# Optimization experiments

Hardware: AMD Instinct MI355X
Metric: run time of the kernel (lower is better)

Reference implementation:

```python
import jax, jax.numpy as jnp
import numpy as np
from jax import lax

SCALES = (1, 4, 16, 64)
EPS = 1e-5
B, S, D, H, R, FF = 4, 1024, 512, 8, 4, 2048
C = D // len(SCALES)  # channels per temporal scale


def _ln(x, g, b):
    mu = jnp.mean(x, -1, keepdims=True)
    var = jnp.mean(jnp.square(x - mu), -1, keepdims=True)
    return (x - mu) * lax.rsqrt(var + EPS) * g + b


def _interp_linear(y, L_out):
    # y: [B, C, L_in]; torch F.interpolate(mode='linear', align_corners=False)
    L_in = y.shape[-1]
    if L_in == L_out:
        return y
    pos = (jnp.arange(L_out, dtype=jnp.float32) + 0.5) * (L_in / L_out) - 0.5
    pos = jnp.clip(pos, 0.0, L_in - 1)
    lo = jnp.floor(pos).astype(jnp.int32)
    hi = jnp.minimum(lo + 1, L_in - 1)
    w = (pos - lo.astype(jnp.float32))
    return y[..., lo] * (1.0 - w) + y[..., hi] * w


def _conv1d(x, w, b, stride):
    # x: [B, Cin, L], w: [Cout, Cin, K]
    y = lax.conv_general_dilated(x, w, window_strides=(stride,), padding='VALID',
                                 dimension_numbers=('NCH', 'OIH', 'NCH'))
    return y + b[None, :, None]


def setup_inputs() -> dict:
    key = jax.random.key(0)
    ks = jax.random.split(key, 40)
    n = lambda k, shp, s=0.02: jax.random.normal(k, shp, jnp.float32) * s
    inp = {}
    inp['x'] = jax.random.normal(ks[0], (B, S, D), jnp.float32)
    inp['resource_mask'] = jax.random.randint(ks[1], (B, S), 0, R, jnp.int32)
    inp['attention_mask'] = jnp.ones((B, S), jnp.int32)
    inp['wq'] = n(ks[2], (D, D)); inp['bq'] = jnp.zeros((D,), jnp.float32)
    inp['wk'] = n(ks[3], (D, D)); inp['bk'] = jnp.zeros((D,), jnp.float32)
    inp['wv'] = n(ks[4], (D, D)); inp['bv'] = jnp.zeros((D,), jnp.float32)
    inp['wo'] = n(ks[5], (D, D)); inp['bo'] = jnp.zeros((D,), jnp.float32)
    inp['rbias'] = jax.random.normal(ks[6], (H, R, R), jnp.float32)
    for i, sc in enumerate(SCALES):
        inp[f'cw{i}'] = n(ks[7 + i], (C, D, sc))
        inp[f'cb{i}'] = jnp.zeros((C,), jnp.float32)
    inp['fw'] = n(ks[12], (D, D)); inp['fb'] = jnp.zeros((D,), jnp.float32)
    inp['ltg'] = jnp.ones((D,), jnp.float32); inp['ltb'] = jnp.zeros((D,), jnp.float32)
    inp['n1g'] = jnp.ones((D,), jnp.float32); inp['n1b'] = jnp.zeros((D,), jnp.float32)
    inp['n2g'] = jnp.ones((D,), jnp.float32); inp['n2b'] = jnp.zeros((D,), jnp.float32)
    inp['fw1'] = n(ks[13], (FF, D)); inp['fb1'] = jnp.zeros((FF,), jnp.float32)
    inp['fw2'] = n(ks[14], (D, FF)); inp['fb2'] = jnp.zeros((D,), jnp.float32)
    inp['n3g'] = jnp.ones((D,), jnp.float32); inp['n3b'] = jnp.zeros((D,), jnp.float32)
    return inp


def reference(x, resource_mask, attention_mask, wq, bq, wk, bk, wv, bv, wo, bo, rbias,
              cw0, cb0, cw1, cb1, cw2, cb2, cw3, cb3, fw, fb, ltg, ltb,
              n1g, n1b, n2g, n2b, fw1, fb1, fw2, fb2, n3g, n3b):
    b_, s_, d_ = x.shape
    dk = d_ // H
    # --- ResourceAwareAttention (dropout = identity in eval) ---
    q = (x @ wq.T + bq).reshape(b_, s_, H, dk).transpose(0, 2, 1, 3)
    k = (x @ wk.T + bk).reshape(b_, s_, H, dk).transpose(0, 2, 1, 3)
    v = (x @ wv.T + bv).reshape(b_, s_, H, dk).transpose(0, 2, 1, 3)
    scores = jnp.einsum('bhid,bhjd->bhij', q, k) / jnp.sqrt(jnp.float32(dk))
    # vectorized resource-bias gather: bias[b,h,i,j] = rbias[h, rm[b,i], rm[b,j]]
    idx_h = jnp.arange(H)[None, :, None, None]
    idx_i = resource_mask[:, None, :, None]
    idx_j = resource_mask[:, None, None, :]
    scores = scores + rbias[idx_h, idx_i, idx_j]
    scores = jnp.where(attention_mask[:, None, None, :] == 0, -1e9, scores)
    attn = jax.nn.softmax(scores, axis=-1)
    o = jnp.einsum('bhij,bhjd->bhid', attn, v).transpose(0, 2, 1, 3).reshape(b_, s_, d_)
    attn_out = o @ wo.T + bo
    x = _ln(x + attn_out, n1g, n1b)
    # --- MultiScaleTemporalEncoder ---
    xc = x.transpose(0, 2, 1)  # [B, D, S]
    convs = ((cw0, cb0), (cw1, cb1), (cw2, cb2), (cw3, cb3))
    outs = []
    for sc, (w, bb) in zip(SCALES, convs):
        y = _conv1d(xc, w, bb, sc)  # [B, C, S/sc]
        outs.append(_interp_linear(y, s_))
    ms = jnp.concatenate(outs, axis=1).transpose(0, 2, 1)  # [B, S, D]
    fused = ms @ fw.T + fb
    temporal = _ln(x + fused, ltg, ltb)
    x = _ln(x + temporal, n2g, n2b)
    # --- FFN ---
    ff = jax.nn.relu(x @ fw1.T + fb1) @ fw2.T + fb2
    return _ln(x + ff, n3g, n3b)
```

## Files before the change

kernel.cpp:

```cpp
#include <hip/hip_runtime.h>
#include <math.h>

constexpr int B_ = 4, S_ = 1024, D_ = 512, H_ = 8, FF_ = 2048;
constexpr int DK_ = 64;
constexpr int C_ = 128;
constexpr int QKVLD = 1536;

typedef __bf16 bf16x8 __attribute__((ext_vector_type(8)));
typedef __bf16 bf16x4 __attribute__((ext_vector_type(4)));
typedef short short4v __attribute__((ext_vector_type(4)));
typedef float floatx4 __attribute__((ext_vector_type(4)));

__device__ __forceinline__ void g2l16(const __bf16* g, __bf16* l) {
  __builtin_amdgcn_global_load_lds(
      (__attribute__((address_space(1))) void*)(unsigned long long)g,
      (__attribute__((address_space(3))) void*)(unsigned int)(unsigned long long)l,
      16, 0, 0);
}

template <bool OUTBF16, bool RELU, bool WRITEVT>
__global__ __launch_bounds__(256, 2) void mgemm(
    const __bf16* __restrict__ A, const __bf16* __restrict__ W,
    const float* __restrict__ bias, void* __restrict__ Yv,
    int M, int N, int K, int ldY, __bf16* __restrict__ VT) {
  __shared__ __bf16 As[2][128 * 64];
  __shared__ __bf16 Bs[2][128 * 64];
  const int tid = threadIdx.x;
  const int wave = tid >> 6, lane = tid & 63;
  const int bm = blockIdx.y * 128, bn = blockIdx.x * 128;

  const int rsub = lane >> 3;
  const int gch = ((lane & 7) ^ rsub) * 8;
  const __bf16* gA = A + (size_t)(bm + wave * 32 + rsub) * K + gch;
  const __bf16* gB = W + (size_t)(bn + wave * 32 + rsub) * K + gch;

  const int mrow = lane & 15, g4 = lane >> 4;
  const int rsw = mrow & 7;
  const int wm = (wave & 1) * 64, wn = (wave >> 1) * 64;

  floatx4 acc[4][4];
#pragma unroll
  for (int mi = 0; mi < 4; mi++)
#pragma unroll
    for (int ni = 0; ni < 4; ni++) acc[mi][ni] = (floatx4){0.f, 0.f, 0.f, 0.f};

  const int nk = K >> 6;
  auto stage = [&](int buf, int kt) {
    const __bf16* ga = gA + (size_t)kt * 64;
    const __bf16* gb = gB + (size_t)kt * 64;
    __bf16* la = &As[buf][wave * 32 * 64];
    __bf16* lb = &Bs[buf][wave * 32 * 64];
#pragma unroll
    for (int i = 0; i < 4; i++) {
      g2l16(ga + (size_t)(i * 8) * K, la + i * 8 * 64);
      g2l16(gb + (size_t)(i * 8) * K, lb + i * 8 * 64);
    }
  };

  stage(0, 0);
  int cur = 0;
  for (int kk = 0; kk < nk; kk++) {
    __syncthreads();
    if (kk + 1 < nk) stage(cur ^ 1, kk + 1);
    const __bf16* Ab = As[cur];
    const __bf16* Bb = Bs[cur];
#pragma unroll
    for (int c = 0; c < 2; c++) {
      const int pc = (((c * 4 + g4) ^ rsw)) * 8;
      bf16x8 af[4], bfr[4];
#pragma unroll
      for (int mi = 0; mi < 4; mi++)
        af[mi] = *(const bf16x8*)(Ab + (wm + mi * 16 + mrow) * 64 + pc);
#pragma unroll
      for (int ni = 0; ni < 4; ni++)
        bfr[ni] = *(const bf16x8*)(Bb + (wn + ni * 16 + mrow) * 64 + pc);
#pragma unroll
      for (int mi = 0; mi < 4; mi++)
#pragma unroll
        for (int ni = 0; ni < 4; ni++)
          acc[mi][ni] = __builtin_amdgcn_mfma_f32_16x16x32_bf16(af[mi], bfr[ni], acc[mi][ni], 0, 0, 0);
    }
    cur ^= 1;
  }

  const int cc = lane & 15;
  const int r0 = (lane >> 4) * 4;
  float bv[4];
#pragma unroll
  for (int ni = 0; ni < 4; ni++) bv[ni] = bias[bn + wn + ni * 16 + cc];
#pragma unroll
  for (int mi = 0; mi < 4; mi++) {
#pragma unroll
    for (int ni = 0; ni < 4; ni++) {
      const int col = bn + wn + ni * 16 + cc;
      if (WRITEVT && col >= 1024) {
        const int h = (col - 1024) >> 6, d = (col - 1024) & 63;
        const int rowb = bm + wm + mi * 16 + r0;
        const int b = rowb >> 10, s = rowb & 1023;
        union { __bf16 hh[4]; unsigned long long u; } w;
#pragma unroll
        for (int i = 0; i < 4; i++) w.hh[i] = (__bf16)(acc[mi][ni][i] + bv[ni]);
        *(unsigned long long*)(VT + (size_t)(b * 8 + h) * 65536 + (size_t)d * 1024 + s) = w.u;
      } else {
#pragma unroll
        for (int i = 0; i < 4; i++) {
          float v = acc[mi][ni][i] + bv[ni];
          if (RELU) v = fmaxf(v, 0.f);
          const size_t row = bm + wm + mi * 16 + r0 + i;
          if (OUTBF16)
            ((__bf16*)Yv)[row * ldY + col] = (__bf16)v;
          else
            ((float*)Yv)[row * ldY + col] = v;
        }
      }
    }
  }
}

template <bool OUTBF16, bool RELU>
__global__ __launch_bounds__(256, 2) void mgemm64(
    const __bf16* __restrict__ A, const __bf16* __restrict__ W,
    const float* __restrict__ bias, void* __restrict__ Yv,
    int M, int N, int K, int ldY) {
  __shared__ __bf16 As[2][64 * 64];
  __shared__ __bf16 Bs[2][64 * 64];
  const int tid = threadIdx.x;
  const int wave = tid >> 6, lane = tid & 63;
  const int bm = blockIdx.y * 64, bn = blockIdx.x * 64;

  const int rsub = lane >> 3;
  const int gch = ((lane & 7) ^ rsub) * 8;
  const __bf16* gA = A + (size_t)(bm + wave * 16 + rsub) * K + gch;
  const __bf16* gB = W + (size_t)(bn + wave * 16 + rsub) * K + gch;

  const int mrow = lane & 15, g4 = lane >> 4;
  const int rsw = mrow & 7;
  const int wm = (wave & 1) * 32, wn = (wave >> 1) * 32;

  floatx4 acc[2][2];
#pragma unroll
  for (int mi = 0; mi < 2; mi++)
#pragma unroll
    for (int ni = 0; ni < 2; ni++) acc[mi][ni] = (floatx4){0.f, 0.f, 0.f, 0.f};

  const int nk = K >> 6;
  auto stage = [&](int buf, int kt) {
    const __bf16* ga = gA + (size_t)kt * 64;
    const __bf16* gb = gB + (size_t)kt * 64;
    __bf16* la = &As[buf][wave * 16 * 64];
    __bf16* lb = &Bs[buf][wave * 16 * 64];
#pragma unroll
    for (int i = 0; i < 2; i++) {
      g2l16(ga + (size_t)(i * 8) * K, la + i * 8 * 64);
      g2l16(gb + (size_t)(i * 8) * K, lb + i * 8 * 64);
    }
  };

  stage(0, 0);
  int cur = 0;
  for (int kk = 0; kk < nk; kk++) {
    __syncthreads();
    if (kk + 1 < nk) stage(cur ^ 1, kk + 1);
    const __bf16* Ab = As[cur];
    const __bf16* Bb = Bs[cur];
#pragma unroll
    for (int c = 0; c < 2; c++) {
      const int pc = (((c * 4 + g4) ^ rsw)) * 8;
      bf16x8 af[2], bfr[2];
#pragma unroll
      for (int mi = 0; mi < 2; mi++)
        af[mi] = *(const bf16x8*)(Ab + (wm + mi * 16 + mrow) * 64 + pc);
#pragma unroll
      for (int ni = 0; ni < 2; ni++)
        bfr[ni] = *(const bf16x8*)(Bb + (wn + ni * 16 + mrow) * 64 + pc);
#pragma unroll
      for (int mi = 0; mi < 2; mi++)
#pragma unroll
        for (int ni = 0; ni < 2; ni++)
          acc[mi][ni] = __builtin_amdgcn_mfma_f32_16x16x32_bf16(af[mi], bfr[ni], acc[mi][ni], 0, 0, 0);
    }
    cur ^= 1;
  }

  const int cc = lane & 15;
  const int r0 = (lane >> 4) * 4;
  float bv[2];
#pragma unroll
  for (int ni = 0; ni < 2; ni++) bv[ni] = bias[bn + wn + ni * 16 + cc];
#pragma unroll
  for (int mi = 0; mi < 2; mi++) {
#pragma unroll
    for (int ni = 0; ni < 2; ni++) {
      const int col = bn + wn + ni * 16 + cc;
#pragma unroll
      for (int i = 0; i < 4; i++) {
        float v = acc[mi][ni][i] + bv[ni];
        if (RELU) v = fmaxf(v, 0.f);
        const size_t row = bm + wm + mi * 16 + r0 + i;
        if (OUTBF16)
          ((__bf16*)Yv)[row * ldY + col] = (__bf16)v;
        else
          ((float*)Yv)[row * ldY + col] = v;
      }
    }
  }
}

__global__ __launch_bounds__(256, 2) void cgemm3(
    const __bf16* __restrict__ A, const __bf16* __restrict__ w4,
    const __bf16* __restrict__ w16, const __bf16* __restrict__ w64,
    const __bf16* __restrict__ w1, const float* __restrict__ cb0,
    float* __restrict__ y1, float* __restrict__ y2, float* __restrict__ y3,
    __bf16* __restrict__ msb) {
  int id = blockIdx.x;
  const __bf16* W;
  float* yseg = nullptr;
  int M, K, bm, k0s;
  bool direct = false;
  if (id < 64) {
    W = w4; yseg = y1; M = 1024; K = 2048;
    bm = (id & 15) * 64; k0s = id >> 4;
  } else if (id < 128) {
    id -= 64;
    W = w16; yseg = y2; M = 256; K = 8192;
    bm = (id & 3) * 64; k0s = id >> 2;
  } else if (id < 192) {
    id -= 128;
    W = w64; yseg = y3; M = 64; K = 32768;
    bm = 0; k0s = id;
  } else {
    id -= 192;
    W = w1; M = 4096; K = 512;
    bm = id * 64; k0s = 0; direct = true;
  }
  const int k0 = k0s * 512;

  __shared__ __bf16 As[2][64 * 32];
  __shared__ __bf16 Bs[2][128 * 32];
  const int tid = threadIdx.x;
  const int wave = tid >> 6, lane = tid & 63;

  const int rs2 = lane >> 2;
  const int ssw2 = (rs2 & 3) ^ ((rs2 >> 2) & 3);
  const int gc2 = ((lane & 3) ^ ssw2) * 8;
  const __bf16* gA = A + (size_t)(bm + wave * 16 + rs2) * K + k0 + gc2;
  const __bf16* gB0 = W + (size_t)(wave * 16 + rs2) * K + k0 + gc2;
  const __bf16* gB1 = W + (size_t)(64 + wave * 16 + rs2) * K + k0 + gc2;

  const int mrow = lane & 15, g4 = lane >> 4;
  const int fsw = (lane & 3) ^ ((lane >> 2) & 3);
  const int fc = (g4 ^ fsw) & 3;

  floatx4 acc[8];
#pragma unroll
  for (int nj = 0; nj < 8; nj++) acc[nj] = (floatx4){0.f, 0.f, 0.f, 0.f};

  auto stage = [&](int buf, int kt) {
    const size_t ko = (size_t)kt * 32;
    g2l16(gA + ko, &As[buf][wave * 16 * 32]);
    g2l16(gB0 + ko, &Bs[buf][wave * 16 * 32]);
    g2l16(gB1 + ko, &Bs[buf][(64 + wave * 16) * 32]);
  };

  stage(0, 0);
  int cur = 0;
  for (int kk = 0; kk < 16; kk++) {
    __syncthreads();
    if (kk + 1 < 16) stage(cur ^ 1, kk + 1);
    bf16x8 af = *(const bf16x8*)(As[cur] + (wave * 16 + mrow) * 32 + fc * 8);
#pragma unroll
    for (int nj = 0; nj < 8; nj++) {
      bf16x8 bfv = *(const bf16x8*)(Bs[cur] + (nj * 16 + mrow) * 32 + fc * 8);
      acc[nj] = __builtin_amdgcn_mfma_f32_16x16x32_bf16(af, bfv, acc[nj], 0, 0, 0);
    }
    cur ^= 1;
  }

  const int cc = lane & 15;
  const int r0 = (lane >> 4) * 4;
  if (direct) {
#pragma unroll
    for (int nj = 0; nj < 8; nj++) {
      const float bb = cb0[nj * 16 + cc];
#pragma unroll
      for (int i = 0; i < 4; i++)
        msb[(size_t)(bm + wave * 16 + r0 + i) * 512 + nj * 16 + cc] =
            (__bf16)(acc[nj][i] + bb);
    }
  } else {
#pragma unroll
    for (int nj = 0; nj < 8; nj++)
#pragma unroll
      for (int i = 0; i < 4; i++)
        atomicAdd(&yseg[(size_t)(bm + wave * 16 + r0 + i) * 128 + nj * 16 + cc],
                  acc[nj][i]);
  }
}

__global__ __launch_bounds__(256) void prep(
    const float* __restrict__ cw1, const float* __restrict__ cw2,
    const float* __restrict__ cw3, __bf16* __restrict__ wt4,
    __bf16* __restrict__ wt16, __bf16* __restrict__ wt64,
    const float* __restrict__ s0, const float* __restrict__ s1,
    const float* __restrict__ s2, const float* __restrict__ s3,
    const float* __restrict__ s4, const float* __restrict__ s5,
    const float* __restrict__ s6, const float* __restrict__ s7,
    const float* __restrict__ s8,
    __bf16* __restrict__ d0, __bf16* __restrict__ d1, __bf16* __restrict__ d2,
    __bf16* __restrict__ d3, __bf16* __restrict__ d4, __bf16* __restrict__ d5,
    __bf16* __restrict__ d6, __bf16* __restrict__ d7, __bf16* __restrict__ d8,
    const float* __restrict__ bq, const float* __restrict__ bk,
    const float* __restrict__ bv, float* __restrict__ bqkv,
    const float* __restrict__ cb1, const float* __restrict__ cb2,
    const float* __restrict__ cb3, float* __restrict__ yall) {
  __shared__ float Ts[4608];
  const int tid = threadIdx.x;
  if (blockIdx.x < 1408) {
    int id = blockIdx.x;
    const float* cw;
    __bf16* wt;
    int lg, c, d0i, TD, L;
    if (id < 128) {
      cw = cw1; wt = wt4; lg = 2; c = id; d0i = 0; TD = 512; L = 2048;
    } else if (id < 384) {
      id -= 128;
      cw = cw2; wt = wt16; lg = 4; c = id >> 1; d0i = (id & 1) * 256; TD = 256; L = 4096;
    } else {
      id -= 384;
      cw = cw3; wt = wt64; lg = 6; c = id >> 3; d0i = (id & 7) * 64; TD = 64; L = 4096;
    }
    const int sc = 1 << lg;
    const int KD = 512 << lg;
    const float* src = cw + (size_t)c * KD + (size_t)d0i * sc;

    for (int f = tid * 4; f < L; f += 1024) {
      const float4 v = *(const float4*)(src + f);
      const float vv[4] = {v.x, v.y, v.z, v.w};
#pragma unroll
      for (int j = 0; j < 4; j++) {
        const int idx = f + j;
        const int dl = idx >> lg, k = idx & (sc - 1);
        Ts[dl * (sc + 1) + k] = vv[j];
      }
    }
    __syncthreads();

    for (int w = tid * 8; w < L; w += 2048) {
      const int kpos = w / TD;
      const int dl0 = w - kpos * TD;
      union { __bf16 hh[8]; bf16x8 v; } u;
#pragma unroll
      for (int j = 0; j < 8; j++)
        u.hh[j] = (__bf16)Ts[(dl0 + j) * (sc + 1) + kpos];
      *(bf16x8*)(wt + (size_t)c * KD + kpos * 512 + d0i + dl0) = u.v;
    }
    return;
  }

  const int qd = (blockIdx.x - 1408) * 256 + tid;
  if (qd < 384) {
    const int i = qd * 4;
    const float* s;
    int off;
    if (i < 512) { s = bq; off = 0; }
    else if (i < 1024) { s = bk; off = 512; }
    else { s = bv; off = 1024; }
    *(float4*)(bqkv + i) = *(const float4*)(s + i - off);
  }
  if (qd < 172032) {
    float bb;
    if (qd < 131072) bb = cb1[qd & 127];
    else if (qd < 163840) bb = cb2[qd & 127];
    else bb = cb3[qd & 127];
    yall[qd] = bb;
  }
  if (qd >= 1392640) return;
  const float* src;
  __bf16* dst;
  int base;
  if (qd < 524288) { src = s0; dst = d0; base = 0; }
  else if (qd < 589824) { src = s1; dst = d1; base = 524288; }
  else if (qd < 655360) { src = s2; dst = d2; base = 589824; }
  else if (qd < 720896) { src = s3; dst = d3; base = 655360; }
  else if (qd < 786432) { src = s4; dst = d4; base = 720896; }
  else if (qd < 851968) { src = s5; dst = d5; base = 786432; }
  else if (qd < 868352) { src = s6; dst = d6; base = 851968; }
  else if (qd < 1130496) { src = s7; dst = d7; base = 868352; }
  else { src = s8; dst = d8; base = 1130496; }
  const int local = qd - base;
  float4 v = *(const float4*)(src + (size_t)local * 4);
  union { __bf16 h[4]; unsigned long long u; } t;
  t.h[0] = (__bf16)v.x; t.h[1] = (__bf16)v.y;
  t.h[2] = (__bf16)v.z; t.h[3] = (__bf16)v.w;
  *(unsigned long long*)(dst + (size_t)local * 4) = t.u;
}

__global__ __launch_bounds__(256) void fattn(
    const __bf16* __restrict__ QKV, const __bf16* __restrict__ VT,
    const float* __restrict__ rbias, const int* __restrict__ rm,
    const int* __restrict__ amask, float* __restrict__ pO,
    float* __restrict__ ml) {
  __shared__ __bf16 Ks[64 * 72];
  __shared__ __bf16 Vs[64 * 72];
  __shared__ float T[4 * 520];

  const int tid = threadIdx.x, wave = tid >> 6, lane = tid & 63;
  const int bh = blockIdx.y, b = bh >> 3, h = bh & 7;
  const int q0 = blockIdx.x * 64;
  const int jh = blockIdx.z;
  const int cc = lane & 15, quad = lane >> 4;

  for (int j = tid; j < 512; j += 256) {
    const int gj = jh * 512 + j;
    const int rv = rm[b * S_ + gj];
    const float mk = amask[b * S_ + gj] ? 1.f : 0.f;
#pragma unroll
    for (int ri = 0; ri < 4; ri++)
      T[ri * 520 + j] = __expf(rbias[h * 16 + ri * 4 + rv]) * mk;
  }

  const int qrow = q0 + wave * 16;
  const int rmi = rm[b * S_ + qrow + cc];
  const float* Trow = T + rmi * 520;

  const __bf16* Qr = QKV + (size_t)(b * S_ + qrow + cc) * QKVLD + h * 64;
  const bf16x8 qb0 = *(const bf16x8*)(Qr + quad * 8);
  const bf16x8 qb1 = *(const bf16x8*)(Qr + 32 + quad * 8);

  floatx4 of[4];
#pragma unroll
  for (int dc = 0; dc < 4; dc++) of[dc] = (floatx4){0.f, 0.f, 0.f, 0.f};
  float mold = -1e30f, l = 0.f;

  const __bf16* Kbase = QKV + (size_t)(b * S_ + jh * 512) * QKVLD + 512 + h * 64;
  const __bf16* Vtbase = VT + (size_t)bh * 65536 + jh * 512;
  const int srow = tid >> 2, sch = tid & 3;

  for (int jt = 0; jt < 8; jt++) {
    const int j0 = jt * 64;
    __syncthreads();
    {
      const __bf16* kg = Kbase + (size_t)(j0 + srow) * QKVLD;
      *(bf16x8*)(Ks + srow * 72 + sch * 8) = *(const bf16x8*)(kg + sch * 8);
      *(bf16x8*)(Ks + srow * 72 + 32 + sch * 8) = *(const bf16x8*)(kg + 32 + sch * 8);
      const __bf16* vg = Vtbase + (size_t)srow * 1024 + j0;
      *(bf16x8*)(Vs + srow * 72 + sch * 8) = *(const bf16x8*)(vg + sch * 8);
      *(bf16x8*)(Vs + srow * 72 + 32 + sch * 8) = *(const bf16x8*)(vg + 32 + sch * 8);
    }
    __syncthreads();

    floatx4 st[4];
#pragma unroll
    for (int js = 0; js < 4; js++) {
      const bf16x8 ka0 = *(const bf16x8*)(Ks + (js * 16 + cc) * 72 + quad * 8);
      const bf16x8 ka1 = *(const bf16x8*)(Ks + (js * 16 + cc) * 72 + 32 + quad * 8);
      floatx4 s = (floatx4){0.f, 0.f, 0.f, 0.f};
      s = __builtin_amdgcn_mfma_f32_16x16x32_bf16(ka0, qb0, s, 0, 0, 0);
      s = __builtin_amdgcn_mfma_f32_16x16x32_bf16(ka1, qb1, s, 0, 0, 0);
      st[js] = s;
    }

    float mxr = st[0][0];
#pragma unroll
    for (int js = 0; js < 4; js++)
#pragma unroll
      for (int i = 0; i < 4; i++) mxr = fmaxf(mxr, st[js][i]);
    mxr = fmaxf(mxr, __shfl_xor(mxr, 16));
    mxr = fmaxf(mxr, __shfl_xor(mxr, 32));
    const float mnew = fmaxf(mold, mxr * 0.125f);
    const float alpha = __expf(mold - mnew);
    mold = mnew;

    float rsum = 0.f;
    short4v pk[4];
#pragma unroll
    for (int js = 0; js < 4; js++) {
      const floatx4 Tv = *(const floatx4*)(Trow + j0 + js * 16 + quad * 4);
      union { __bf16 hh[4]; short4v s4; } u;
#pragma unroll
      for (int i = 0; i < 4; i++) {
        const float p = __expf(fmaf(st[js][i], 0.125f, -mnew)) * Tv[i];
        rsum += p;
        u.hh[i] = (__bf16)p;
      }
      pk[js] = u.s4;
    }
    rsum += __shfl_xor(rsum, 16);
    rsum += __shfl_xor(rsum, 32);
    l = l * alpha + rsum;

#pragma unroll
    for (int dc = 0; dc < 4; dc++)
#pragma unroll
      for (int i = 0; i < 4; i++) of[dc][i] *= alpha;

#pragma unroll
    for (int dc = 0; dc < 4; dc++) {
#pragma unroll
      for (int js = 0; js < 4; js++) {
        union { bf16x4 v; short4v s4; } va;
        va.v = *(const bf16x4*)(Vs + (dc * 16 + cc) * 72 + js * 16 + quad * 4);
        of[dc] = __builtin_amdgcn_mfma_f32_16x16x16bf16_1k(va.s4, pk[js], of[dc], 0, 0, 0);
      }
    }
  }

  const int pidx = (bh * 16 + blockIdx.x) * 2 + jh;
  const int lrow = wave * 16 + cc;
  float* po = pO + (size_t)pidx * 4096 + lrow * 64;
#pragma unroll
  for (int dc = 0; dc < 4; dc++)
    *(floatx4*)(po + dc * 16 + quad * 4) = of[dc];
  if (quad == 0) {
    ml[pidx * 64 + lrow] = mold;
    ml[65536 + pidx * 64 + lrow] = l;
  }
}

__global__ void fmerge(const float* __restrict__ pO, const float* __restrict__ ml,
                       __bf16* __restrict__ O) {
  const int idx = blockIdx.x * 256 + threadIdx.x;
  if (idx >= 2097152) return;
  const int d = idx & 63;
  const int row = (idx >> 6) & 63;
  const int qb = (idx >> 12) & 15;
  const int bh = idx >> 16;
  const int p0 = (bh * 16 + qb) * 2;
  const float m0 = ml[p0 * 64 + row], m1 = ml[(p0 + 1) * 64 + row];
  const float l0 = ml[65536 + p0 * 64 + row], l1 = ml[65536 + (p0 + 1) * 64 + row];
  const float mm = fmaxf(m0, m1);
  const float w0 = __expf(m0 - mm), w1 = __expf(m1 - mm);
  const float o = (w0 * pO[(size_t)p0 * 4096 + row * 64 + d] +
                   w1 * pO[(size_t)(p0 + 1) * 4096 + row * 64 + d]) /
                  (w0 * l0 + w1 * l1);
  const int b = bh >> 3, h = bh & 7;
  O[(size_t)(b * S_ + qb * 64 + row) * D_ + h * 64 + d] = (__bf16)o;
}

__global__ __launch_bounds__(256) void add_ln_kernel(
    const float* __restrict__ xa, const float* __restrict__ xb,
    const float* __restrict__ g, const float* __restrict__ be,
    float* __restrict__ out, __bf16* __restrict__ outb) {
  const int row = (blockIdx.x * 256 + threadIdx.x) >> 6;
  const int lane = threadIdx.x & 63;
  const float* pa = xa + (size_t)row * D_;
  const float* pb = xb + (size_t)row * D_;
  float v[8];
  float sum = 0.f;
#pragma unroll
  for (int i = 0; i < 8; i++) {
    int dd = lane + 64 * i;
    v[i] = pa[dd] + pb[dd];
    sum += v[i];
  }
#pragma unroll
  for (int off = 32; off; off >>= 1) sum += __shfl_xor(sum, off);
  const float mu = sum * (1.f / D_);
  float vs = 0.f;
#pragma unroll
  for (int i = 0; i < 8; i++) { float t = v[i] - mu; vs += t * t; }
#pragma unroll
  for (int off = 32; off; off >>= 1) vs += __shfl_xor(vs, off);
  const float inv = rsqrtf(vs * (1.f / D_) + 1e-5f);
  float* po = out + (size_t)row * D_;
#pragma unroll
  for (int i = 0; i < 8; i++) {
    int dd = lane + 64 * i;
    float o = (v[i] - mu) * inv * g[dd] + be[dd];
    po[dd] = o;
    if (outb) outb[(size_t)row * D_ + dd] = (__bf16)o;
  }
}

__global__ __launch_bounds__(256) void ln_chain_kernel(
    const float* __restrict__ x1, const float* __restrict__ fused,
    const float* __restrict__ ltg, const float* __restrict__ ltb,
    const float* __restrict__ n2g, const float* __restrict__ n2b,
    float* __restrict__ out, __bf16* __restrict__ outb) {
  const int row = (blockIdx.x * 256 + threadIdx.x) >> 6;
  const int lane = threadIdx.x & 63;
  const float* p1 = x1 + (size_t)row * D_;
  const float* pf = fused + (size_t)row * D_;
  float xv[8], u[8];
  float sum = 0.f;
#pragma unroll
  for (int i = 0; i < 8; i++) {
    int dd = lane + 64 * i;
    xv[i] = p1[dd];
    u[i] = xv[i] + pf[dd];
    sum += u[i];
  }
#pragma unroll
  for (int off = 32; off; off >>= 1) sum += __shfl_xor(sum, off);
  float mu = sum * (1.f / D_);
  float vs = 0.f;
#pragma unroll
  for (int i = 0; i < 8; i++) { float t = u[i] - mu; vs += t * t; }
#pragma unroll
  for (int off = 32; off; off >>= 1) vs += __shfl_xor(vs, off);
  float inv = rsqrtf(vs * (1.f / D_) + 1e-5f);
  float sum2 = 0.f;
#pragma unroll
  for (int i = 0; i < 8; i++) {
    int dd = lane + 64 * i;
    float t = (u[i] - mu) * inv * ltg[dd] + ltb[dd];
    u[i] = xv[i] + t;
    sum2 += u[i];
  }
#pragma unroll
  for (int off = 32; off; off >>= 1) sum2 += __shfl_xor(sum2, off);
  float mu2 = sum2 * (1.f / D_);
  float vs2 = 0.f;
#pragma unroll
  for (int i = 0; i < 8; i++) { float t = u[i] - mu2; vs2 += t * t; }
#pragma unroll
  for (int off = 32; off; off >>= 1) vs2 += __shfl_xor(vs2, off);
  float inv2 = rsqrtf(vs2 * (1.f / D_) + 1e-5f);
  float* po = out + (size_t)row * D_;
#pragma unroll
  for (int i = 0; i < 8; i++) {
    int dd = lane + 64 * i;
    float o = (u[i] - mu2) * inv2 * n2g[dd] + n2b[dd];
    po[dd] = o;
    outb[(size_t)row * D_ + dd] = (__bf16)o;
  }
}

__global__ void interp_kernel(const float* __restrict__ y1, const float* __restrict__ y2,
                              const float* __restrict__ y3, __bf16* __restrict__ ms) {
  int idx = blockIdx.x * 256 + threadIdx.x;
  if (idx >= B_ * S_ * 3 * C_) return;
  int c3 = idx % (3 * C_);
  int rest = idx / (3 * C_);
  int s = rest % S_, b = rest / S_;
  int i = c3 >> 7;
  int c = c3 & 127;
  int Lin = (i == 0) ? 256 : (i == 1) ? 64 : 16;
  const float* y = (i == 0) ? y1 : (i == 1) ? y2 : y3;
  float pos = (s + 0.5f) * ((float)Lin / S_) - 0.5f;
  pos = fminf(fmaxf(pos, 0.f), (float)(Lin - 1));
  int lo = (int)floorf(pos);
  int hi = min(lo + 1, Lin - 1);
  float w = pos - (float)lo;
  const float* ybase = y + ((size_t)(b * Lin + lo)) * 128 + c;
  float vlo = ybase[0];
  float vhi = ybase[(size_t)(hi - lo) * 128];
  ms[((size_t)b * S_ + s) * D_ + C_ + c3] = (__bf16)(vlo * (1.f - w) + vhi * w);
}

extern "C" void kernel_launch(void* const* d_in, const int* in_sizes, int n_in,
                              void* d_out, int out_size, void* d_ws, size_t ws_size,
                              hipStream_t stream) {
  const float* x   = (const float*)d_in[0];
  const int* rm    = (const int*)d_in[1];
  const int* am    = (const int*)d_in[2];
  const float* wq  = (const float*)d_in[3];
  const float* bq  = (const float*)d_in[4];
  const float* wk  = (const float*)d_in[5];
  const float* bk  = (const float*)d_in[6];
  const float* wv  = (const float*)d_in[7];
  const float* bv  = (const float*)d_in[8];
  const float* wo  = (const float*)d_in[9];
  const float* bo  = (const float*)d_in[10];
  const float* rbias = (const float*)d_in[11];
  const float* cw0 = (const float*)d_in[12];
  const float* cb0 = (const float*)d_in[13];
  const float* cw1 = (const float*)d_in[14];
  const float* cb1 = (const float*)d_in[15];
  const float* cw2 = (const float*)d_in[16];
  const float* cb2 = (const float*)d_in[17];
  const float* cw3 = (const float*)d_in[18];
  const float* cb3 = (const float*)d_in[19];
  const float* fw  = (const float*)d_in[20];
  const float* fb  = (const float*)d_in[21];
  const float* ltg = (const float*)d_in[22];
  const float* ltb = (const float*)d_in[23];
  const float* n1g = (const float*)d_in[24];
  const float* n1b = (const float*)d_in[25];
  const float* n2g = (const float*)d_in[26];
  const float* n2b = (const float*)d_in[27];
  const float* fw1 = (const float*)d_in[28];
  const float* fb1 = (const float*)d_in[29];
  const float* fw2 = (const float*)d_in[30];
  const float* fb2 = (const float*)d_in[31];
  const float* n3g = (const float*)d_in[32];
  const float* n3b = (const float*)d_in[33];

  float* ws = (float*)d_ws;
  __bf16* wqkvb = (__bf16*)(ws + 0);
  __bf16* wob   = (__bf16*)(ws + 393216);
  __bf16* fwb   = (__bf16*)(ws + 524288);
  __bf16* cw0b  = (__bf16*)(ws + 655360);
  __bf16* fw1b  = (__bf16*)(ws + 688128);
  __bf16* fw2b  = (__bf16*)(ws + 1212416);
  __bf16* xb    = (__bf16*)(ws + 1835008);
  __bf16* qkv   = (__bf16*)(ws + 2883584);
  __bf16* attnb = (__bf16*)(ws + 6029312);
  float*  x1    = ws + 7077888;
  __bf16* x1b   = (__bf16*)(ws + 9175040);
  float*  scr   = ws + 10223616;
  float*  x2    = ws + 12320768;
  __bf16* x2b   = (__bf16*)(ws + 14417920);
  __bf16* msb   = (__bf16*)(ws + 15466496);
  float*  y1    = ws + 16515072;
  float*  y2    = ws + 16646144;
  float*  y3    = ws + 16678912;
  float*  bqkv  = ws + 16687104;
  __bf16* wt4b  = (__bf16*)(ws + 16689152);
  __bf16* wt16b = (__bf16*)(ws + 16820224);
  __bf16* wt64b = (__bf16*)(ws + 17344512);
  __bf16* VT    = (__bf16*)(ws + 10223616);
  float*  pO    = ws + 12320768;
  float*  ml    = ws + 7077888;
  __bf16* ffh   = (__bf16*)(ws + 2883584);

  dim3 blk(256);

  prep<<<6848, blk, 0, stream>>>(
      cw1, cw2, cw3, wt4b, wt16b, wt64b,
      x, wq, wk, wv, wo, fw, cw0, fw1, fw2,
      xb, wqkvb, wqkvb + 262144, wqkvb + 524288, wob, fwb, cw0b, fw1b, fw2b,
      bq, bk, bv, bqkv, cb1, cb2, cb3, y1);

  mgemm<true, false, true><<<dim3(12, 32), blk, 0, stream>>>(
      xb, wqkvb, bqkv, qkv, 4096, 1536, 512, QKVLD, VT);

  fattn<<<dim3(16, 32, 2), blk, 0, stream>>>(qkv, VT, rbias, rm, am, pO, ml);
  fmerge<<<8192, blk, 0, stream>>>(pO, ml, attnb);

  mgemm64<false, false><<<dim3(8, 64), blk, 0, stream>>>(
      attnb, wob, bo, scr, 4096, 512, 512, 512);
  add_ln_kernel<<<1024, blk, 0, stream>>>(x, scr, n1g, n1b, x1, x1b);

  cgemm3<<<256, blk, 0, stream>>>(x1b, wt4b, wt16b, wt64b, cw0b, cb0, y1, y2, y3, msb);
  interp_kernel<<<6144, blk, 0, stream>>>(y1, y2, y3, msb);

  mgemm64<false, false><<<dim3(8, 64), blk, 0, stream>>>(
      msb, fwb, fb, scr, 4096, 512, 512, 512);
  ln_chain_kernel<<<1024, blk, 0, stream>>>(x1, scr, ltg, ltb, n2g, n2b, x2, x2b);

  mgemm<true, true, false><<<dim3(16, 32), blk, 0, stream>>>(
      x2b, fw1b, fb1, ffh, 4096, 2048, 512, 2048, nullptr);
  mgemm64<false, false><<<dim3(8, 64), blk, 0, stream>>>(
      ffh, fw2b, fb2, scr, 4096, 512, 2048, 512);
  add_ln_kernel<<<1024, blk, 0, stream>>>(x2, scr, n3g, n3b, (float*)d_out, nullptr);
}
```

Baseline: 279.5 us.

## Drop split-KV attention merge, add XCD-aware block swizzle and MFMA priority hints

Attention no longer splits the key range across two blocks. Each block now walks all 1024 keys and writes normalized bf16 output directly, which removes the fmerge kernel and the fp32 partial-output round trip. Block indices in the GEMMs and attention are remapped so consecutive tiles land on the same XCD, aiming for better L2 reuse. s_setprio is raised around the MFMA sections. The trade-off is half as many attention blocks (512 instead of 1024), so less parallelism and longer per-block serial loops.

Measured after the change: 273.9 us. 1.02x faster.

```diff
diff --git a/kernel.cpp b/kernel.cpp
--- a/kernel.cpp
+++ b/kernel.cpp
@@ -16,6 +16,10 @@
       (__attribute__((address_space(1))) void*)(unsigned long long)g,
       (__attribute__((address_space(3))) void*)(unsigned int)(unsigned long long)l,
       16, 0, 0);
+}
+
+__device__ __forceinline__ int xcd_swz(int lin, int nwg) {
+  return (lin & 7) * (nwg >> 3) + (lin >> 3);
 }
 
 template <bool OUTBF16, bool RELU, bool WRITEVT>
@@ -27,7 +31,10 @@
   __shared__ __bf16 Bs[2][128 * 64];
   const int tid = threadIdx.x;
   const int wave = tid >> 6, lane = tid & 63;
-  const int bm = blockIdx.y * 128, bn = blockIdx.x * 128;
+  const int nwg = gridDim.x * gridDim.y;
+  const int lin = blockIdx.y * gridDim.x + blockIdx.x;
+  const int swz = xcd_swz(lin, nwg);
+  const int bm = (swz / gridDim.x) * 128, bn = (swz % gridDim.x) * 128;
 
   const int rsub = lane >> 3;
   const int gch = ((lane & 7) ^ rsub) * 8;
@@ -126,7 +133,10 @@
   __shared__ __bf16 Bs[2][64 * 64];
   const int tid = threadIdx.x;
   const int wave = tid >> 6, lane = tid & 63;
-  const int bm = blockIdx.y * 64, bn = blockIdx.x * 64;
+  const int nwg = gridDim.x * gridDim.y;
+  const int lin = blockIdx.y * gridDim.x + blockIdx.x;
+  const int swz = xcd_swz(lin, nwg);
+  const int bm = (swz / gridDim.x) * 64, bn = (swz % gridDim.x) * 64;
 
   const int rsub = lane >> 3;
   const int gch = ((lane & 7) ^ rsub) * 8;
@@ -398,30 +408,32 @@
 __global__ __launch_bounds__(256) void fattn(
     const __bf16* __restrict__ QKV, const __bf16* __restrict__ VT,
     const float* __restrict__ rbias, const int* __restrict__ rm,
-    const int* __restrict__ amask, float* __restrict__ pO,
-    float* __restrict__ ml) {
+    const int* __restrict__ amask, __bf16* __restrict__ O) {
   __shared__ __bf16 Ks[64 * 72];
   __shared__ __bf16 Vs[64 * 72];
-  __shared__ float T[4 * 520];
+  __shared__ float T[4 * 1032];
 
   const int tid = threadIdx.x, wave = tid >> 6, lane = tid & 63;
-  const int bh = blockIdx.y, b = bh >> 3, h = bh & 7;
-  const int q0 = blockIdx.x * 64;
-  const int jh = blockIdx.z;
+  const int nwg = gridDim.x * gridDim.y;
+  const int lin = blockIdx.y * gridDim.x + blockIdx.x;
+  const int swz = xcd_swz(lin, nwg);
+  const int qb = swz % gridDim.x;
+  const int bh = swz / gridDim.x;
+  const int b = bh >> 3, h = bh & 7;
+  const int q0 = qb * 64;
   const int cc = lane & 15, quad = lane >> 4;
 
-  for (int j = tid; j < 512; j += 256) {
-    const int gj = jh * 512 + j;
-    const int rv = rm[b * S_ + gj];
-    const float mk = amask[b * S_ + gj] ? 1.f : 0.f;
+  for (int j = tid; j < 1024; j += 256) {
+    const int rv = rm[b * S_ + j];
+    const float mk = amask[b * S_ + j] ? 1.f : 0.f;
 #pragma unroll
     for (int ri = 0; ri < 4; ri++)
-      T[ri * 520 + j] = __expf(rbias[h * 16 + ri * 4 + rv]) * mk;
+      T[ri * 1032 + j] = __expf(rbias[h * 16 + ri * 4 + rv]) * mk;
   }
 
   const int qrow = q0 + wave * 16;
   const int rmi = rm[b * S_ + qrow + cc];
-  const float* Trow = T + rmi * 520;
+  const float* Trow = T + rmi * 1032;
 
   const __bf16* Qr = QKV + (size_t)(b * S_ + qrow + cc) * QKVLD + h * 64;
   const bf16x8 qb0 = *(const bf16x8*)(Qr + quad * 8);
@@ -432,11 +444,11 @@
   for (int dc = 0; dc < 4; dc++) of[dc] = (floatx4){0.f, 0.f, 0.f, 0.f};
   float mold = -1e30f, l = 0.f;
 
-  const __bf16* Kbase = QKV + (size_t)(b * S_ + jh * 512) * QKVLD + 512 + h * 64;
-  const __bf16* Vtbase = VT + (size_t)bh * 65536 + jh * 512;
+  const __bf16* Kbase = QKV + (size_t)(b * S_) * QKVLD + 512 + h * 64;
+  const __bf16* Vtbase = VT + (size_t)bh * 65536;
   const int srow = tid >> 2, sch = tid & 3;
 
-  for (int jt = 0; jt < 8; jt++) {
+  for (int jt = 0; jt < 16; jt++) {
     const int j0 = jt * 64;
     __syncthreads();
     {
@@ -450,6 +462,7 @@
     __syncthreads();
 
     floatx4 st[4];
+    __builtin_amdgcn_s_setprio(1);
 #pragma unroll
     for (int js = 0; js < 4; js++) {
       const bf16x8 ka0 = *(const bf16x8*)(Ks + (js * 16 + cc) * 72 + quad * 8);
@@ -459,6 +472,7 @@
       s = __builtin_amdgcn_mfma_f32_16x16x32_bf16(ka1, qb1, s, 0, 0, 0);
       st[js] = s;
     }
+    __builtin_amdgcn_s_setprio(0);
 
     float mxr = st[0][0];
 #pragma unroll
@@ -494,6 +508,7 @@
 #pragma unroll
       for (int i = 0; i < 4; i++) of[dc][i] *= alpha;
 
+    __builtin_amdgcn_s_setprio(1);
 #pragma unroll
     for (int dc = 0; dc < 4; dc++) {
 #pragma unroll
@@ -503,38 +518,18 @@
         of[dc] = __builtin_amdgcn_mfma_f32_16x16x16bf16_1k(va.s4, pk[js], of[dc], 0, 0, 0);
       }
     }
-  }
-
-  const int pidx = (bh * 16 + blockIdx.x) * 2 + jh;
-  const int lrow = wave * 16 + cc;
-  float* po = pO + (size_t)pidx * 4096 + lrow * 64;
-#pragma unroll
-  for (int dc = 0; dc < 4; dc++)
-    *(floatx4*)(po + dc * 16 + quad * 4) = of[dc];
-  if (quad == 0) {
-    ml[pidx * 64 + lrow] = mold;
-    ml[65536 + pidx * 64 + lrow] = l;
-  }
-}
-
-__global__ void fmerge(const float* __restrict__ pO, const float* __restrict__ ml,
-                       __bf16* __restrict__ O) {
-  const int idx = blockIdx.x * 256 + threadIdx.x;
-  if (idx >= 2097152) return;
-  const int d = idx & 63;
-  const int row = (idx >> 6) & 63;
-  const int qb = (idx >> 12) & 15;
-  const int bh = idx >> 16;
-  const int p0 = (bh * 16 + qb) * 2;
-  const float m0 = ml[p0 * 64 + row], m1 = ml[(p0 + 1) * 64 + row];
-  const float l0 = ml[65536 + p0 * 64 + row], l1 = ml[65536 + (p0 + 1) * 64 + row];
-  const float mm = fmaxf(m0, m1);
-  const float w0 = __expf(m0 - mm), w1 = __expf(m1 - mm);
-  const float o = (w0 * pO[(size_t)p0 * 4096 + row * 64 + d] +
-                   w1 * pO[(size_t)(p0 + 1) * 4096 + row * 64 + d]) /
-                  (w0 * l0 + w1 * l1);
-  const int b = bh >> 3, h = bh & 7;
-  O[(size_t)(b * S_ + qb * 64 + row) * D_ + h * 64 + d] = (__bf16)o;
+    __builtin_amdgcn_s_setprio(0);
+  }
+
+  const float invl = 1.f / l;
+  __bf16* po = O + (size_t)(b * S_ + qrow + cc) * D_ + h * 64;
+#pragma unroll
+  for (int dc = 0; dc < 4; dc++) {
+    union { __bf16 hh[4]; unsigned long long u; } w;
+#pragma unroll
+    for (int i = 0; i < 4; i++) w.hh[i] = (__bf16)(of[dc][i] * invl);
+    *(unsigned long long*)(po + dc * 16 + quad * 4) = w.u;
+  }
 }
 
 __global__ __launch_bounds__(256) void add_ln_kernel(
@@ -710,8 +705,6 @@
   __bf16* wt16b = (__bf16*)(ws + 16820224);
   __bf16* wt64b = (__bf16*)(ws + 17344512);
   __bf16* VT    = (__bf16*)(ws + 10223616);
-  float*  pO    = ws + 12320768;
-  float*  ml    = ws + 7077888;
   __bf16* ffh   = (__bf16*)(ws + 2883584);
 
   dim3 blk(256);
@@ -725,8 +718,7 @@
   mgemm<true, false, true><<<dim3(12, 32), blk, 0, stream>>>(
       xb, wqkvb, bqkv, qkv, 4096, 1536, 512, QKVLD, VT);
 
-  fattn<<<dim3(16, 32, 2), blk, 0, stream>>>(qkv, VT, rbias, rm, am, pO, ml);
-  fmerge<<<8192, blk, 0, stream>>>(pO, ml, attnb);
+  fattn<<<dim3(16, 32), blk, 0, stream>>>(qkv, VT, rbias, rm, am, attnb);
 
   mgemm64<false, false><<<dim3(8, 64), blk, 0, stream>>>(
       attnb, wob, bo, scr, 4096, 512, 512, 512);
```
